# Optimization experiments

Hardware: AMD Instinct MI355X
Metric: run time of the kernel (lower is better)

## Reference

```python
import jax, jax.numpy as jnp
import numpy as np

K_OUTLIER = 16   # decomposition_topk default k
Q = 127.0        # int8 symmetric quant scale


def _quantize(mat):
    # per-row abs-max symmetric quantization; torch .to(int8) truncates toward
    # zero, which matches XLA's float->int convert semantics.
    mmax = jnp.max(jnp.abs(mat), axis=-1)                      # [...,]
    q = (mat * (Q / mmax)[..., None]).astype(jnp.int8)
    return q, mmax


def setup_inputs() -> dict:
    key = jax.random.key(0)
    k1, k2, k3 = jax.random.split(key, 3)
    B, I, O = 4096, 2048, 2048
    x = jax.random.normal(k1, (B, I), jnp.float32)
    weight = jax.random.normal(k2, (O, I), jnp.float32) * 0.02  # nn.Linear convention [out, in]
    bias = jax.random.normal(k3, (O,), jnp.float32) * 0.02
    return {"x": x, "weight": weight, "bias": bias}


def reference(x, weight, bias):
    # --- weight-side prep (done once in __init__ in the torch module) ---
    col_max = jnp.max(jnp.abs(weight), axis=0)                 # [I] abs-max per input column
    idx = jax.lax.top_k(col_max, K_OUTLIER)[1]                 # [k] outlier input columns
    w_unq = weight[:, idx].T                                   # [k, O] fp outlier weights
    w0 = weight.at[:, idx].set(0.0)                            # zero outlier columns
    w_q, w_max = _quantize(w0)                                 # int8 [O, I], fp [O]

    # --- activation side ---
    x_unq = x[:, idx]                                          # [B, k]
    x1 = x.at[:, idx].set(0.0)
    x_q, x_max = _quantize(x1)                                 # int8 [B, I], fp [B]

    # int8 matmul accumulated in int32 (MatMulInteger), then dequantize
    res_q_i32 = jnp.matmul(x_q.astype(jnp.int32), w_q.T.astype(jnp.int32))  # [B, O]
    mx = x_max[:, None] * w_max[None, :]                       # outer product of row/col maxes
    res_q = (res_q_i32.astype(jnp.float32) / (Q * Q)).astype(jnp.float16).astype(jnp.float32) * mx

    # fp outlier path + bias
    res_unq = x_unq @ w_unq + bias                             # [B, O]
    return res_q + res_unq
```

## Files before the change

kernel.cpp:

```cpp
#include <hip/hip_runtime.h>
#include <hip/hip_fp16.h>
#include <stdint.h>

#define I_DIM 2048
#define O_DIM 2048
#define B_DIM 4096
#define KOUT 16

typedef int i32x4 __attribute__((ext_vector_type(4)));
typedef float f32x4 __attribute__((ext_vector_type(4)));
typedef _Float16 f16x8 __attribute__((ext_vector_type(8)));

#define TO_LDS(p) ((__attribute__((address_space(3))) void*)(p))
#define TO_GLB(p) ((const __attribute__((address_space(1))) void*)(p))

__global__ void colmax_kernel(const float* __restrict__ W, unsigned* __restrict__ cm) {
  int j = blockIdx.x * 256 + threadIdx.x;
  int i0 = blockIdx.y * 64;
  float m = 0.0f;
  const float* p = W + (size_t)i0 * I_DIM + j;
  for (int i = 0; i < 64; ++i)
    m = fmaxf(m, fabsf(p[(size_t)i * I_DIM]));
  atomicMax(cm + j, __float_as_uint(m));
}

__global__ void topk_kernel(const unsigned* __restrict__ cm, int* __restrict__ idx,
                            float* __restrict__ keep) {
  int t = threadIdx.x;
  const float4* c4 = (const float4*)cm;
  float4 a = c4[t * 2], b = c4[t * 2 + 1];
  float v[8] = {a.x, a.y, a.z, a.w, b.x, b.y, b.z, b.w};
  for (int j = t; j < I_DIM; j += 256) keep[j] = 1.0f;
  __shared__ float wm_[4];
  __shared__ int wi_[4];
  __shared__ int sel;
  for (int k = 0; k < KOUT; ++k) {
    float m = v[0]; int mi = 0;
#pragma unroll
    for (int r = 1; r < 8; ++r) if (v[r] > m) { m = v[r]; mi = r; }
    int gi = t * 8 + mi;
#pragma unroll
    for (int s = 32; s; s >>= 1) {
      float om = __shfl_down(m, s);
      int oi = __shfl_down(gi, s);
      if (om > m) { m = om; gi = oi; }
    }
    if ((t & 63) == 0) { wm_[t >> 6] = m; wi_[t >> 6] = gi; }
    __syncthreads();
    if (t == 0) {
      float bm = wm_[0]; int bi = wi_[0];
      for (int w2 = 1; w2 < 4; ++w2) if (wm_[w2] > bm) { bm = wm_[w2]; bi = wi_[w2]; }
      idx[k] = bi; keep[bi] = 0.0f; sel = bi;
    }
    __syncthreads();
    if (t == (sel >> 3)) v[sel & 7] = -1.0f;
  }
}

__global__ __launch_bounds__(256) void quant_kernel(
    const float* __restrict__ X, const float* __restrict__ W,
    const float* __restrict__ keep, const int* __restrict__ idx,
    signed char* __restrict__ xq, signed char* __restrict__ wq,
    float* __restrict__ xmax, float* __restrict__ wmax,
    _Float16* __restrict__ xunqh,
    _Float16* __restrict__ wunqh) {
  int b = blockIdx.x;
  int t = threadIdx.x;
  bool isW = b < O_DIM;
  int r = isW ? b : (b - O_DIM);
  const float* src = isW ? (W + (size_t)r * I_DIM) : (X + (size_t)r * I_DIM);
  const float4* s4 = (const float4*)src;
  const float4* k4 = (const float4*)keep;
  float4 v0 = s4[t], v1 = s4[t + 256];
  float4 k0 = k4[t], k1 = k4[t + 256];
  v0.x *= k0.x; v0.y *= k0.y; v0.z *= k0.z; v0.w *= k0.w;
  v1.x *= k1.x; v1.y *= k1.y; v1.z *= k1.z; v1.w *= k1.w;
  float m = fmaxf(fmaxf(fmaxf(fabsf(v0.x), fabsf(v0.y)), fmaxf(fabsf(v0.z), fabsf(v0.w))),
                  fmaxf(fmaxf(fabsf(v1.x), fabsf(v1.y)), fmaxf(fabsf(v1.z), fabsf(v1.w))));
#pragma unroll
  for (int s = 32; s; s >>= 1) m = fmaxf(m, __shfl_xor(m, s));
  __shared__ float red[4];
  if ((t & 63) == 0) red[t >> 6] = m;
  __syncthreads();
  m = fmaxf(fmaxf(red[0], red[1]), fmaxf(red[2], red[3]));
  float sc = 127.0f / m;
  unsigned p0 = (unsigned char)(signed char)(int)(v0.x * sc)
              | ((unsigned)(unsigned char)(signed char)(int)(v0.y * sc) << 8)
              | ((unsigned)(unsigned char)(signed char)(int)(v0.z * sc) << 16)
              | ((unsigned)(unsigned char)(signed char)(int)(v0.w * sc) << 24);
  unsigned p1 = (unsigned char)(signed char)(int)(v1.x * sc)
              | ((unsigned)(unsigned char)(signed char)(int)(v1.y * sc) << 8)
              | ((unsigned)(unsigned char)(signed char)(int)(v1.z * sc) << 16)
              | ((unsigned)(unsigned char)(signed char)(int)(v1.w * sc) << 24);
  unsigned* qout = (unsigned*)(isW ? (wq + (size_t)r * I_DIM) : (xq + (size_t)r * I_DIM));
  qout[t] = p0;
  qout[t + 256] = p1;
  if (t == 0) { if (isW) wmax[r] = m; else xmax[r] = m; }
  if (t < KOUT) {
    float ov = src[idx[t]];
    _Float16* u = isW ? (wunqh + (size_t)r * 32) : (xunqh + (size_t)r * 32);
    u[t] = (_Float16)ov;
    u[t + KOUT] = (_Float16)0.0f;
  }
}

__global__ __launch_bounds__(256) void gemm_kernel(
    const signed char* __restrict__ Aq,
    const signed char* __restrict__ Bq,
    const float* __restrict__ xmaxg,
    const float* __restrict__ wmaxg,
    const _Float16* __restrict__ xunqh,
    const _Float16* __restrict__ wunqh,
    const float* __restrict__ biasg,
    float* __restrict__ out) {
  constexpr int N = O_DIM, K = I_DIM;
  __shared__ __align__(16) signed char smem[16384];
  signed char* As = smem;
  signed char* Bs = smem + 8192;

  const int tid = threadIdx.x;
  const int lane = tid & 63;
  const int wave = tid >> 6;
  const int wm = (wave & 1) * 64;
  const int wn = (wave >> 1) * 64;
  const int m0 = blockIdx.y * 128;
  const int n0 = blockIdx.x * 128;
  const int row0 = tid >> 2;
  const int col0 = ((((tid & 3) - (row0 >> 1)) & 3) * 16);
  const int fm = lane & 15;
  const int q = lane >> 4;

  i32x4 acc[4][4] = {};

  for (int kt = 0; kt < K; kt += 64) {
    const signed char* ga0 = Aq + (size_t)(m0 + row0) * K + kt + col0;
    const signed char* gb0 = Bq + (size_t)(n0 + row0) * K + kt + col0;
    __builtin_amdgcn_global_load_lds(TO_GLB(ga0), TO_LDS(As + wave * 1024), 16, 0, 0);
    __builtin_amdgcn_global_load_lds(TO_GLB(ga0 + (size_t)64 * K), TO_LDS(As + 4096 + wave * 1024), 16, 0, 0);
    __builtin_amdgcn_global_load_lds(TO_GLB(gb0), TO_LDS(Bs + wave * 1024), 16, 0, 0);
    __builtin_amdgcn_global_load_lds(TO_GLB(gb0 + (size_t)64 * K), TO_LDS(Bs + 4096 + wave * 1024), 16, 0, 0);
    __syncthreads();
    i32x4 af[4], bf[4];
#pragma unroll
    for (int i = 0; i < 4; ++i) {
      int r = wm + i * 16 + fm;
      af[i] = *(const i32x4*)(As + r * 64 + (((q + (r >> 1)) & 3) << 4));
    }
#pragma unroll
    for (int i = 0; i < 4; ++i) {
      int r = wn + i * 16 + fm;
      bf[i] = *(const i32x4*)(Bs + r * 64 + (((q + (r >> 1)) & 3) << 4));
    }
#pragma unroll
    for (int i = 0; i < 4; ++i)
#pragma unroll
      for (int j = 0; j < 4; ++j)
        acc[i][j] = __builtin_amdgcn_mfma_i32_16x16x64_i8(af[i], bf[j], acc[i][j], 0, 0, 0);
    __syncthreads();
  }

  f16x8 afh[4], bfh[4];
#pragma unroll
  for (int i = 0; i < 4; ++i)
    afh[i] = *(const f16x8*)(xunqh + (size_t)(m0 + wm + i * 16 + fm) * 32 + q * 8);
#pragma unroll
  for (int j = 0; j < 4; ++j)
    bfh[j] = *(const f16x8*)(wunqh + (size_t)(n0 + wn + j * 16 + fm) * 32 + q * 8);

#pragma unroll
  for (int i = 0; i < 4; ++i) {
    f32x4 xmv = *(const f32x4*)(xmaxg + m0 + wm + i * 16 + q * 4);
#pragma unroll
    for (int j = 0; j < 4; ++j) {
      int cl = n0 + wn + j * 16 + fm;
      float wmv = wmaxg[cl];
      float bv = biasg[cl];
      f32x4 c;
#pragma unroll
      for (int r = 0; r < 4; ++r) {
        float v = (float)acc[i][j][r] / 16129.0f;
        v = __half2float(__float2half(v));
        c[r] = v * (xmv[r] * wmv) + bv;
      }
      c = __builtin_amdgcn_mfma_f32_16x16x32_f16(afh[i], bfh[j], c, 0, 0, 0);
#pragma unroll
      for (int r = 0; r < 4; ++r)
        out[(size_t)(m0 + wm + i * 16 + q * 4 + r) * N + cl] = c[r];
    }
  }
}

extern "C" void kernel_launch(void* const* d_in, const int* in_sizes, int n_in,
                              void* d_out, int out_size, void* d_ws, size_t ws_size,
                              hipStream_t stream) {
  const float* x    = (const float*)d_in[0];
  const float* w    = (const float*)d_in[1];
  const float* bias = (const float*)d_in[2];
  float* out = (float*)d_out;
  char* ws = (char*)d_ws;

  unsigned* cm     = (unsigned*)(ws + 0);
  int* idx         = (int*)(ws + 8192);
  float* keep      = (float*)(ws + 8320);
  float* w_max     = (float*)(ws + 16512);
  float* x_max     = (float*)(ws + 24704);
  _Float16* x_unqh = (_Float16*)(ws + 41088);
  _Float16* w_unqh = (_Float16*)(ws + 303232);
  signed char* w_q = (signed char*)(ws + 434304);
  signed char* x_q = (signed char*)(ws + 4628608);

  hipMemsetAsync(cm, 0, 8192, stream);
  colmax_kernel<<<dim3(8, 32), 256, 0, stream>>>(w, cm);
  topk_kernel<<<1, 256, 0, stream>>>(cm, idx, keep);
  quant_kernel<<<O_DIM + B_DIM, 256, 0, stream>>>(x, w, keep, idx, x_q, w_q,
                                                  x_max, w_max, x_unqh, w_unqh);
  gemm_kernel<<<dim3(O_DIM / 128, B_DIM / 128), 256, 0, stream>>>(
      x_q, w_q, x_max, w_max, x_unqh, w_unqh, bias, out);
}
```

Before: 148.8 us.

## Use 32x32 int8 MFMA with 128-wide K tiles and drop colmax atomics

```diff
diff --git a/kernel.cpp b/kernel.cpp
--- a/kernel.cpp
+++ b/kernel.cpp
@@ -8,28 +8,36 @@
 #define KOUT 16
 
 typedef int i32x4 __attribute__((ext_vector_type(4)));
+typedef int i32x16 __attribute__((ext_vector_type(16)));
 typedef float f32x4 __attribute__((ext_vector_type(4)));
+typedef float f32x16 __attribute__((ext_vector_type(16)));
 typedef _Float16 f16x8 __attribute__((ext_vector_type(8)));
 
 #define TO_LDS(p) ((__attribute__((address_space(3))) void*)(p))
 #define TO_GLB(p) ((const __attribute__((address_space(1))) void*)(p))
 
-__global__ void colmax_kernel(const float* __restrict__ W, unsigned* __restrict__ cm) {
+__global__ void colmax_kernel(const float* __restrict__ W, float* __restrict__ cmp) {
   int j = blockIdx.x * 256 + threadIdx.x;
   int i0 = blockIdx.y * 64;
   float m = 0.0f;
   const float* p = W + (size_t)i0 * I_DIM + j;
+#pragma unroll 8
   for (int i = 0; i < 64; ++i)
     m = fmaxf(m, fabsf(p[(size_t)i * I_DIM]));
-  atomicMax(cm + j, __float_as_uint(m));
-}
-
-__global__ void topk_kernel(const unsigned* __restrict__ cm, int* __restrict__ idx,
+  cmp[blockIdx.y * I_DIM + j] = m;
+}
+
+__global__ void topk_kernel(const float* __restrict__ cmp, int* __restrict__ idx,
                             float* __restrict__ keep) {
   int t = threadIdx.x;
-  const float4* c4 = (const float4*)cm;
-  float4 a = c4[t * 2], b = c4[t * 2 + 1];
-  float v[8] = {a.x, a.y, a.z, a.w, b.x, b.y, b.z, b.w};
+  float v[8];
+#pragma unroll
+  for (int u = 0; u < 8; ++u) v[u] = 0.0f;
+  for (int rc = 0; rc < 32; ++rc) {
+    const float* row = cmp + rc * I_DIM;
+#pragma unroll
+    for (int u = 0; u < 8; ++u) v[u] = fmaxf(v[u], row[u * 256 + t]);
+  }
   for (int j = t; j < I_DIM; j += 256) keep[j] = 1.0f;
   __shared__ float wm_[4];
   __shared__ int wi_[4];
@@ -37,8 +45,8 @@
   for (int k = 0; k < KOUT; ++k) {
     float m = v[0]; int mi = 0;
 #pragma unroll
-    for (int r = 1; r < 8; ++r) if (v[r] > m) { m = v[r]; mi = r; }
-    int gi = t * 8 + mi;
+    for (int u = 1; u < 8; ++u) if (v[u] > m) { m = v[u]; mi = u; }
+    int gi = mi * 256 + t;
 #pragma unroll
     for (int s = 32; s; s >>= 1) {
       float om = __shfl_down(m, s);
@@ -53,7 +61,7 @@
       idx[k] = bi; keep[bi] = 0.0f; sel = bi;
     }
     __syncthreads();
-    if (t == (sel >> 3)) v[sel & 7] = -1.0f;
+    if (t == (sel & 255)) v[sel >> 8] = -1.0f;
   }
 }
 
@@ -98,9 +106,8 @@
   if (t == 0) { if (isW) wmax[r] = m; else xmax[r] = m; }
   if (t < KOUT) {
     float ov = src[idx[t]];
-    _Float16* u = isW ? (wunqh + (size_t)r * 32) : (xunqh + (size_t)r * 32);
+    _Float16* u = isW ? (wunqh + (size_t)r * KOUT) : (xunqh + (size_t)r * KOUT);
     u[t] = (_Float16)ov;
-    u[t + KOUT] = (_Float16)0.0f;
   }
 }
 
@@ -114,78 +121,98 @@
     const float* __restrict__ biasg,
     float* __restrict__ out) {
   constexpr int N = O_DIM, K = I_DIM;
-  __shared__ __align__(16) signed char smem[16384];
+  __shared__ __align__(16) signed char smem[32768];
   signed char* As = smem;
-  signed char* Bs = smem + 8192;
+  signed char* Bs = smem + 16384;
 
   const int tid = threadIdx.x;
   const int lane = tid & 63;
   const int wave = tid >> 6;
+  const int h = lane >> 5;
+  const int ln31 = lane & 31;
   const int wm = (wave & 1) * 64;
   const int wn = (wave >> 1) * 64;
   const int m0 = blockIdx.y * 128;
   const int n0 = blockIdx.x * 128;
-  const int row0 = tid >> 2;
-  const int col0 = ((((tid & 3) - (row0 >> 1)) & 3) * 16);
-  const int fm = lane & 15;
-  const int q = lane >> 4;
-
-  i32x4 acc[4][4] = {};
-
-  for (int kt = 0; kt < K; kt += 64) {
-    const signed char* ga0 = Aq + (size_t)(m0 + row0) * K + kt + col0;
-    const signed char* gb0 = Bq + (size_t)(n0 + row0) * K + kt + col0;
-    __builtin_amdgcn_global_load_lds(TO_GLB(ga0), TO_LDS(As + wave * 1024), 16, 0, 0);
-    __builtin_amdgcn_global_load_lds(TO_GLB(ga0 + (size_t)64 * K), TO_LDS(As + 4096 + wave * 1024), 16, 0, 0);
-    __builtin_amdgcn_global_load_lds(TO_GLB(gb0), TO_LDS(Bs + wave * 1024), 16, 0, 0);
-    __builtin_amdgcn_global_load_lds(TO_GLB(gb0 + (size_t)64 * K), TO_LDS(Bs + 4096 + wave * 1024), 16, 0, 0);
-    __syncthreads();
-    i32x4 af[4], bf[4];
-#pragma unroll
-    for (int i = 0; i < 4; ++i) {
-      int r = wm + i * 16 + fm;
-      af[i] = *(const i32x4*)(As + r * 64 + (((q + (r >> 1)) & 3) << 4));
-    }
-#pragma unroll
-    for (int i = 0; i < 4; ++i) {
-      int r = wn + i * 16 + fm;
-      bf[i] = *(const i32x4*)(Bs + r * 64 + (((q + (r >> 1)) & 3) << 4));
-    }
-#pragma unroll
-    for (int i = 0; i < 4; ++i)
-#pragma unroll
-      for (int j = 0; j < 4; ++j)
-        acc[i][j] = __builtin_amdgcn_mfma_i32_16x16x64_i8(af[i], bf[j], acc[i][j], 0, 0, 0);
-    __syncthreads();
-  }
-
-  f16x8 afh[4], bfh[4];
-#pragma unroll
-  for (int i = 0; i < 4; ++i)
-    afh[i] = *(const f16x8*)(xunqh + (size_t)(m0 + wm + i * 16 + fm) * 32 + q * 8);
-#pragma unroll
-  for (int j = 0; j < 4; ++j)
-    bfh[j] = *(const f16x8*)(wunqh + (size_t)(n0 + wn + j * 16 + fm) * 32 + q * 8);
-
-#pragma unroll
-  for (int i = 0; i < 4; ++i) {
-    f32x4 xmv = *(const f32x4*)(xmaxg + m0 + wm + i * 16 + q * 4);
-#pragma unroll
-    for (int j = 0; j < 4; ++j) {
-      int cl = n0 + wn + j * 16 + fm;
-      float wmv = wmaxg[cl];
-      float bv = biasg[cl];
-      f32x4 c;
-#pragma unroll
-      for (int r = 0; r < 4; ++r) {
-        float v = (float)acc[i][j][r] / 16129.0f;
-        v = __half2float(__float2half(v));
-        c[r] = v * (xmv[r] * wmv) + bv;
+
+  const signed char* srcA[4];
+  const signed char* srcB[4];
+#pragma unroll
+  for (int s = 0; s < 4; ++s) {
+    int f = (s * 4 + wave) * 64 + lane;
+    int r = f >> 3;
+    int g = (f & 7) ^ (r & 7);
+    srcA[s] = Aq + (size_t)(m0 + r) * K + g * 16;
+    srcB[s] = Bq + (size_t)(n0 + r) * K + g * 16;
+  }
+
+  const int rA0 = wm + ln31, rA1 = rA0 + 32;
+  const int rB0 = wn + ln31, rB1 = rB0 + 32;
+  const int oA0 = rA0 * 128, sA0 = rA0 & 7;
+  const int oA1 = rA1 * 128, sA1 = rA1 & 7;
+  const int oB0 = rB0 * 128, sB0 = rB0 & 7;
+  const int oB1 = rB1 * 128, sB1 = rB1 & 7;
+
+  f16x8 afh[2], bfh[2];
+#pragma unroll
+  for (int i = 0; i < 2; ++i)
+    afh[i] = *(const f16x8*)(xunqh + (size_t)(m0 + wm + i * 32 + ln31) * KOUT + h * 8);
+#pragma unroll
+  for (int j = 0; j < 2; ++j)
+    bfh[j] = *(const f16x8*)(wunqh + (size_t)(n0 + wn + j * 32 + ln31) * KOUT + h * 8);
+
+  i32x16 acc[2][2] = {};
+
+  for (int kt = 0; kt < K; kt += 128) {
+#pragma unroll
+    for (int s = 0; s < 4; ++s) {
+      __builtin_amdgcn_global_load_lds(TO_GLB(srcA[s] + kt), TO_LDS(As + (s * 4 + wave) * 1024), 16, 0, 0);
+      __builtin_amdgcn_global_load_lds(TO_GLB(srcB[s] + kt), TO_LDS(Bs + (s * 4 + wave) * 1024), 16, 0, 0);
+    }
+    __syncthreads();
+#pragma unroll
+    for (int st = 0; st < 4; ++st) {
+      int lc = st * 2 + h;
+      i32x4 a0 = *(const i32x4*)(As + oA0 + ((lc ^ sA0) << 4));
+      i32x4 a1 = *(const i32x4*)(As + oA1 + ((lc ^ sA1) << 4));
+      i32x4 b0 = *(const i32x4*)(Bs + oB0 + ((lc ^ sB0) << 4));
+      i32x4 b1 = *(const i32x4*)(Bs + oB1 + ((lc ^ sB1) << 4));
+      acc[0][0] = __builtin_amdgcn_mfma_i32_32x32x32_i8(a0, b0, acc[0][0], 0, 0, 0);
+      acc[0][1] = __builtin_amdgcn_mfma_i32_32x32x32_i8(a0, b1, acc[0][1], 0, 0, 0);
+      acc[1][0] = __builtin_amdgcn_mfma_i32_32x32x32_i8(a1, b0, acc[1][0], 0, 0, 0);
+      acc[1][1] = __builtin_amdgcn_mfma_i32_32x32x32_i8(a1, b1, acc[1][1], 0, 0, 0);
+    }
+    __syncthreads();
+  }
+
+  const float recip = 1.0f / 16129.0f;
+#pragma unroll
+  for (int i = 0; i < 2; ++i) {
+#pragma unroll
+    for (int j = 0; j < 2; ++j) {
+      int col = n0 + wn + j * 32 + ln31;
+      float wmv = wmaxg[col];
+      float bv = biasg[col];
+      f32x16 c;
+#pragma unroll
+      for (int g = 0; g < 4; ++g) {
+        int rbase = m0 + wm + i * 32 + g * 8 + h * 4;
+        f32x4 xmv = *(const f32x4*)(xmaxg + rbase);
+#pragma unroll
+        for (int r = 0; r < 4; ++r) {
+          float v = (float)acc[i][j][g * 4 + r] * recip;
+          v = __half2float(__float2half(v));
+          c[g * 4 + r] = v * (xmv[r] * wmv) + bv;
+        }
       }
-      c = __builtin_amdgcn_mfma_f32_16x16x32_f16(afh[i], bfh[j], c, 0, 0, 0);
-#pragma unroll
-      for (int r = 0; r < 4; ++r)
-        out[(size_t)(m0 + wm + i * 16 + q * 4 + r) * N + cl] = c[r];
+      c = __builtin_amdgcn_mfma_f32_32x32x16_f16(afh[i], bfh[j], c, 0, 0, 0);
+#pragma unroll
+      for (int g = 0; g < 4; ++g) {
+        int rbase = m0 + wm + i * 32 + g * 8 + h * 4;
+#pragma unroll
+        for (int r = 0; r < 4; ++r)
+          out[(size_t)(rbase + r) * N + col] = c[g * 4 + r];
+      }
     }
   }
 }
@@ -199,19 +226,18 @@
   float* out = (float*)d_out;
   char* ws = (char*)d_ws;
 
-  unsigned* cm     = (unsigned*)(ws + 0);
-  int* idx         = (int*)(ws + 8192);
-  float* keep      = (float*)(ws + 8320);
-  float* w_max     = (float*)(ws + 16512);
-  float* x_max     = (float*)(ws + 24704);
-  _Float16* x_unqh = (_Float16*)(ws + 41088);
-  _Float16* w_unqh = (_Float16*)(ws + 303232);
-  signed char* w_q = (signed char*)(ws + 434304);
-  signed char* x_q = (signed char*)(ws + 4628608);
-
-  hipMemsetAsync(cm, 0, 8192, stream);
-  colmax_kernel<<<dim3(8, 32), 256, 0, stream>>>(w, cm);
-  topk_kernel<<<1, 256, 0, stream>>>(cm, idx, keep);
+  float* cm_part   = (float*)(ws + 0);
+  int* idx         = (int*)(ws + 262144);
+  float* keep      = (float*)(ws + 262272);
+  float* w_max     = (float*)(ws + 270464);
+  float* x_max     = (float*)(ws + 278656);
+  _Float16* x_unqh = (_Float16*)(ws + 295040);
+  _Float16* w_unqh = (_Float16*)(ws + 426112);
+  signed char* w_q = (signed char*)(ws + 491648);
+  signed char* x_q = (signed char*)(ws + 4685952);
+
+  colmax_kernel<<<dim3(8, 32), 256, 0, stream>>>(w, cm_part);
+  topk_kernel<<<1, 256, 0, stream>>>(cm_part, idx, keep);
   quant_kernel<<<O_DIM + B_DIM, 256, 0, stream>>>(x, w, keep, idx, x_q, w_q,
                                                   x_max, w_max, x_unqh, w_unqh);
   gemm_kernel<<<dim3(O_DIM / 128, B_DIM / 128), 256, 0, stream>>>(
```

Result: no change. 149.3 us (+0.3%).
